# Kernel optimization log

Measured on AMD Instinct MI355X. Metric: run time of the kernel, lower is better.

The kernel has to match this reference:

```python
import jax, jax.numpy as jnp
import numpy as np

B, T, E, H = 1, 2048, 2048, 32
D = E // H  # head_dim = 64


def alibi_bias(n_heads, t_q, t_k, dtype):
    # slopes: 2^(-8*(h+1)/n_heads) for power-of-two head counts
    slopes = jnp.power(2.0, -8.0 * jnp.arange(1, n_heads + 1, dtype=jnp.float32) / n_heads)
    i = jnp.arange(t_q)[:, None] + (t_k - t_q)  # absolute query positions
    j = jnp.arange(t_k)[None, :]
    rel = (j - i).astype(dtype)                 # [t_q, t_k], <=0 on/below diagonal
    return (slopes[:, None, None] * rel).astype(dtype)  # [H, t_q, t_k]


def setup_inputs() -> dict:
    key = jax.random.key(0)
    kx, kq, kk, kv, ko = jax.random.split(key, 5)
    s = E ** -0.5
    x = jax.random.normal(kx, (B, T, E), dtype=jnp.float32)
    Wq = jax.random.normal(kq, (E, E), dtype=jnp.float32) * s
    Wk = jax.random.normal(kk, (D, E), dtype=jnp.float32) * s
    Wv = jax.random.normal(kv, (D, E), dtype=jnp.float32) * s
    Wo = jax.random.normal(ko, (E, E), dtype=jnp.float32) * s
    # causal mask: True where attention is disallowed (j > i)
    attention_mask = jnp.triu(jnp.ones((T, T), dtype=bool), k=1)[None, None]  # [1,1,T,T]
    return {"x": x, "Wq": Wq, "Wk": Wk, "Wv": Wv, "Wo": Wo, "attention_mask": attention_mask}


def reference(x, Wq, Wk, Wv, Wo, attention_mask):
    b, t, _ = x.shape
    scale = D ** -0.5
    q = (x @ Wq.T).reshape(b, t, H, D).transpose(0, 2, 1, 3)  # [b,H,t,D]
    k = x @ Wk.T                                              # [b,t,D] (single KV head)
    v = x @ Wv.T                                              # [b,t,D]
    attn = jnp.einsum('bhtd,bsd->bhts', q * scale, k)         # [b,H,t,t]
    attn = attn + alibi_bias(H, t, t, attn.dtype)[None]
    attn = jnp.where(attention_mask, jnp.asarray(-10000.0, attn.dtype), attn)
    w = jax.nn.softmax(attn, axis=-1)
    out = jnp.einsum('bhts,bsd->bhtd', w, v)                  # [b,H,t,D]
    out = out.transpose(0, 2, 1, 3).reshape(b, t, E)
    return out @ Wo.T
```

## Files before the change

kernel.cpp:

```cpp
#include <hip/hip_runtime.h>
#include <stdint.h>

typedef __bf16 bf16;
typedef __bf16 bf16x4 __attribute__((ext_vector_type(4)));
typedef __bf16 bf16x8 __attribute__((ext_vector_type(8)));
typedef short short4v __attribute__((ext_vector_type(4)));
typedef float floatx4 __attribute__((ext_vector_type(4)));

#define MFMA32(a, b, c) __builtin_amdgcn_mfma_f32_16x16x32_bf16((a), (b), (c), 0, 0, 0)

__device__ __forceinline__ floatx4 mfma16(bf16x4 a, bf16x4 b, floatx4 c) {
  return __builtin_amdgcn_mfma_f32_16x16x16bf16_1k(
      __builtin_bit_cast(short4v, a), __builtin_bit_cast(short4v, b), c, 0, 0, 0);
}

__device__ __forceinline__ void gload16(const void* g, void* l) {
  __builtin_amdgcn_global_load_lds(
      (const __attribute__((address_space(1))) void*)g,
      (__attribute__((address_space(3))) void*)l, 16, 0, 0);
}

__device__ __forceinline__ bf16x8 load8(const float* p) {
  float4 lo = *(const float4*)p;
  float4 hi = *(const float4*)(p + 4);
  bf16x8 r;
  r[0] = (bf16)lo.x; r[1] = (bf16)lo.y; r[2] = (bf16)lo.z; r[3] = (bf16)lo.w;
  r[4] = (bf16)hi.x; r[5] = (bf16)hi.y; r[6] = (bf16)hi.z; r[7] = (bf16)hi.w;
  return r;
}

__global__ __launch_bounds__(256) void conv3(const float* __restrict__ a, bf16* __restrict__ ab,
                                             const float* __restrict__ b, bf16* __restrict__ bb,
                                             const float* __restrict__ c, bf16* __restrict__ cb) {
  const int i = blockIdx.x * 256 + threadIdx.x;
  const float* src = blockIdx.y == 0 ? a : (blockIdx.y == 1 ? b : c);
  bf16* dst = blockIdx.y == 0 ? ab : (blockIdx.y == 1 ? bb : cb);
  ((bf16x8*)dst)[i] = load8(src + (size_t)i * 8);
}

__global__ __launch_bounds__(256) void pack_kv(const float* __restrict__ Kf,
                                               const float* __restrict__ Vf,
                                               bf16* __restrict__ Kb,
                                               bf16* __restrict__ Vtb) {
  int i = blockIdx.x * 256 + threadIdx.x;
  if (i < 2048 * 64) {
    Kb[i] = (bf16)Kf[i];
    const int t = i >> 6, d = i & 63;
    Vtb[(size_t)d * 2048 + t] = (bf16)Vf[i];
  }
}

template <typename TC>
__global__ __launch_bounds__(256) void gemm_bt_a(const bf16* __restrict__ A,
                                                 const bf16* __restrict__ B,
                                                 TC* __restrict__ C,
                                                 int M, int N, int K) {
  __shared__ __align__(16) bf16 As[2][64 * 32];
  __shared__ __align__(16) bf16 Bs[2][128 * 32];
  const int tid = threadIdx.x;
  const int wave = tid >> 6, lane = tid & 63;
  const int quad = lane >> 4, l16 = lane & 15;
  const int m0 = blockIdx.y * 64, n0 = blockIdx.x * 128;
  const int wm = (wave >> 1) * 32, wn = (wave & 1) * 64;

  floatx4 acc[2][4];
#pragma unroll
  for (int i = 0; i < 2; i++)
#pragma unroll
    for (int j = 0; j < 4; j++) acc[i][j] = (floatx4)0.f;

  const int srow = tid >> 2, scol = (tid & 3) * 8;
  const bf16* Ap = A + (size_t)(m0 + srow) * K + scol;
  const bf16* Bp = B + (size_t)(n0 + srow) * K + scol;

  auto stage = [&](int k0, int buf) {
    gload16(Ap + k0, (char*)As[buf] + tid * 16);
    gload16(Bp + k0, (char*)Bs[buf] + tid * 16);
    gload16(Bp + (size_t)64 * K + k0, (char*)Bs[buf] + 4096 + tid * 16);
  };
  auto compute = [&](int buf) {
    bf16x8 af[2], bfr[4];
#pragma unroll
    for (int mt = 0; mt < 2; mt++)
      af[mt] = *(const bf16x8*)(&As[buf][(wm + mt * 16 + l16) * 32 + quad * 8]);
#pragma unroll
    for (int nt = 0; nt < 4; nt++)
      bfr[nt] = *(const bf16x8*)(&Bs[buf][(wn + nt * 16 + l16) * 32 + quad * 8]);
#pragma unroll
    for (int mt = 0; mt < 2; mt++)
#pragma unroll
      for (int nt = 0; nt < 4; nt++)
        acc[mt][nt] = MFMA32(af[mt], bfr[nt], acc[mt][nt]);
  };

  stage(0, 0);
  for (int k0 = 0; k0 < K; k0 += 64) {
    __syncthreads();
    if (k0 + 32 < K) stage(k0 + 32, 1);
    compute(0);
    __syncthreads();
    if (k0 + 64 < K) stage(k0 + 64, 0);
    compute(1);
  }

#pragma unroll
  for (int mt = 0; mt < 2; mt++) {
#pragma unroll
    for (int nt = 0; nt < 4; nt++) {
      const int col = n0 + wn + nt * 16 + l16;
      const int row = m0 + wm + mt * 16 + quad * 4;
#pragma unroll
      for (int r = 0; r < 4; r++)
        C[(size_t)(row + r) * N + col] = (TC)acc[mt][nt][r];
    }
  }
}

__global__ __launch_bounds__(256) void kv_gemm(const bf16* __restrict__ xb,
                                               const float* __restrict__ Wk,
                                               const float* __restrict__ Wv,
                                               float* __restrict__ Kf,
                                               float* __restrict__ Vf) {
  __shared__ __align__(16) bf16 As[128 * 40];
  __shared__ __align__(16) bf16 Bs[128 * 40];
  const int tid = threadIdx.x;
  const int wave = tid >> 6, lane = tid & 63;
  const int quad = lane >> 4, l16 = lane & 15;
  const int m0 = blockIdx.y * 128;
  const int kbeg = blockIdx.x * 256, kend = kbeg + 256;
  const int wm = (wave >> 1) * 64, wn = (wave & 1) * 64;

  floatx4 acc[4][4];
#pragma unroll
  for (int i = 0; i < 4; i++)
#pragma unroll
    for (int j = 0; j < 4; j++) acc[i][j] = (floatx4)0.f;

  const int sr = tid >> 2, sc = (tid & 3) * 8;

  for (int k0 = kbeg; k0 < kend; k0 += 32) {
    __syncthreads();
#pragma unroll
    for (int rr = 0; rr < 2; rr++) {
      const int row = sr + rr * 64;
      *(bf16x8*)(&As[row * 40 + sc]) =
          *(const bf16x8*)(&xb[(size_t)(m0 + row) * 2048 + k0 + sc]);
      const float* bsrc = (row < 64) ? &Wk[(size_t)row * 2048 + k0 + sc]
                                     : &Wv[(size_t)(row - 64) * 2048 + k0 + sc];
      *(bf16x8*)(&Bs[row * 40 + sc]) = load8(bsrc);
    }
    __syncthreads();

    bf16x8 af[4], bfr[4];
#pragma unroll
    for (int mt = 0; mt < 4; mt++)
      af[mt] = *(const bf16x8*)(&As[(wm + mt * 16 + l16) * 40 + quad * 8]);
#pragma unroll
    for (int nt = 0; nt < 4; nt++)
      bfr[nt] = *(const bf16x8*)(&Bs[(wn + nt * 16 + l16) * 40 + quad * 8]);
#pragma unroll
    for (int mt = 0; mt < 4; mt++)
#pragma unroll
      for (int nt = 0; nt < 4; nt++)
        acc[mt][nt] = MFMA32(af[mt], bfr[nt], acc[mt][nt]);
  }

#pragma unroll
  for (int mt = 0; mt < 4; mt++) {
#pragma unroll
    for (int nt = 0; nt < 4; nt++) {
      const int col = wn + nt * 16 + l16;
      const int row = m0 + wm + mt * 16 + quad * 4;
      float* dst = (col < 64) ? &Kf[(size_t)row * 64 + col]
                              : &Vf[(size_t)row * 64 + (col - 64)];
#pragma unroll
      for (int r = 0; r < 4; r++) atomicAdd(dst + (size_t)r * 64, acc[mt][nt][r]);
    }
  }
}

__global__ __launch_bounds__(1024) void attn_kernel(const bf16* __restrict__ Q,
                                                    const bf16* __restrict__ Kb,
                                                    const bf16* __restrict__ Vtb,
                                                    bf16* __restrict__ O) {
  __shared__ __align__(16) char smem[65536];
  bf16* const Ksm = (bf16*)smem;
  bf16* const Vsm = (bf16*)(smem + 32768);
  float* const comb = (float*)smem;

  const int tid = threadIdx.x;
  const int wq = tid >> 6;
  const int grp = wq >> 3;
  const int wrow = wq & 7;
  const int lane = tid & 63;
  const int quad = lane >> 4, l16 = lane & 15;
  const int h = blockIdx.y;
  const int t = (blockIdx.y < 16) ? (15 - blockIdx.x) : blockIdx.x;
  const float scale2 = 0.125f * 1.44269504f;
  const float slope2 = exp2f(-0.25f * (float)(h + 1)) * 1.44269504f;

  float cq[4];
#pragma unroll
  for (int r = 0; r < 4; r++) cq[r] = slope2 * (float)(quad * 4 + r);
  const float s16 = slope2 * 16.f;
  const bf16x4 ones = {(bf16)1.f, (bf16)1.f, (bf16)1.f, (bf16)1.f};

  const int qi = t * 128 + wrow * 16 + l16;
  bf16x8 qf[2];
#pragma unroll
  for (int kk = 0; kk < 2; kk++)
    qf[kk] = *(const bf16x8*)(&Q[(size_t)qi * 2048 + h * 64 + kk * 32 + quad * 8]);

  floatx4 oacc[4];
#pragma unroll
  for (int dt = 0; dt < 4; dt++) oacc[dt] = (floatx4)0.f;
  floatx4 lacc = (floatx4)0.f;

  const int end = 2 * t + 2;
  const int lo_key = t * 128 - (int)(44.f / slope2);
  const int lo_t = (lo_key <= 0) ? 0 : (lo_key >> 6);
  const int n = (end - lo_t + 1) >> 1;
  const int base = lo_t + grp * n;
  const int kt_last = end - 1;
  const int qw0 = t * 128 + wrow * 16;

  const int tg = tid & 511;
  const int r0 = tg >> 3, sl = tg & 7;
  const int wsw = ((sl ^ (r0 & 7)) << 3);
  const int sx = l16 & 7;

  int kn = min(base, kt_last) * 64;
  bf16x8 kreg = *(const bf16x8*)(&Kb[(size_t)(kn + r0) * 64 + sl * 8]);
  bf16x8 vreg = *(const bf16x8*)(&Vtb[(size_t)r0 * 2048 + kn + sl * 8]);

  for (int i = 0; i < n; i++) {
    const int kt = base + i;
    const int bofs = (grp * 2 + (i & 1)) * 4096;
    *(bf16x8*)(&Ksm[bofs + r0 * 64 + wsw]) = kreg;
    *(bf16x8*)(&Vsm[bofs + r0 * 64 + wsw]) = vreg;
    __syncthreads();
    if (i + 1 < n) {
      const int kn2 = min(kt + 1, kt_last) * 64;
      kreg = *(const bf16x8*)(&Kb[(size_t)(kn2 + r0) * 64 + sl * 8]);
      vreg = *(const bf16x8*)(&Vtb[(size_t)r0 * 2048 + kn2 + sl * 8]);
    }
    const int k0 = kt * 64;
    if (kt >= end) continue;
    if (k0 > qw0 + 15) continue;
    if ((float)(qw0 - k0 - 63) * slope2 > 44.f) continue;

    const bf16* ks = Ksm + bofs;
    const bf16* vs = Vsm + bofs;

    floatx4 s[4];
#pragma unroll
    for (int mt = 0; mt < 4; mt++) s[mt] = (floatx4)0.f;
#pragma unroll
    for (int kk = 0; kk < 2; kk++) {
#pragma unroll
      for (int mt = 0; mt < 4; mt++) {
        bf16x8 kf = *(const bf16x8*)(
            &ks[(mt * 16 + l16) * 64 + (((kk * 4 + quad) ^ sx) << 3)]);
        s[mt] = MFMA32(kf, qf[kk], s[mt]);
      }
    }

    const float base0 = slope2 * (float)(k0 - qi);
    bf16x4 pb[4];
    if (k0 + 63 <= qw0) {
      float b = base0;
#pragma unroll
      for (int mt = 0; mt < 4; mt++) {
        bf16x4 tb;
#pragma unroll
        for (int r = 0; r < 4; r++)
          tb[r] = (bf16)exp2f(__builtin_fmaf(s[mt][r], scale2, b + cq[r]));
        pb[mt] = tb;
        b += s16;
      }
    } else {
      const int qloc = qi - k0;
      float b = base0;
#pragma unroll
      for (int mt = 0; mt < 4; mt++) {
        bf16x4 tb;
#pragma unroll
        for (int r = 0; r < 4; r++) {
          const int moff = mt * 16 + quad * 4 + r;
          const float p = exp2f(__builtin_fmaf(s[mt][r], scale2, b + cq[r]));
          tb[r] = (moff <= qloc) ? (bf16)p : (bf16)0.f;
        }
        pb[mt] = tb;
        b += s16;
      }
    }

#pragma unroll
    for (int mt = 0; mt < 4; mt++) {
      lacc = mfma16(ones, pb[mt], lacc);
#pragma unroll
      for (int dt = 0; dt < 4; dt++) {
        const int slot = 2 * mt + (quad >> 1);
        const bf16x4 va = *(const bf16x4*)(
            &vs[(dt * 16 + l16) * 64 + ((slot ^ sx) << 3) + (quad & 1) * 4]);
        oacc[dt] = mfma16(va, pb[mt], oacc[dt]);
      }
    }
  }

  __syncthreads();
  if (grp == 1) {
    float* c = comb + (size_t)(wrow * 64 + lane) * 17;
#pragma unroll
    for (int dt = 0; dt < 4; dt++)
#pragma unroll
      for (int r = 0; r < 4; r++) c[dt * 4 + r] = oacc[dt][r];
    c[16] = lacc[0];
  }
  __syncthreads();
  if (grp == 0) {
    const float* c = comb + (size_t)(wrow * 64 + lane) * 17;
    const float linv = 1.0f / (lacc[0] + c[16]);
#pragma unroll
    for (int dt = 0; dt < 4; dt++) {
      bf16x4 ob;
#pragma unroll
      for (int r = 0; r < 4; r++)
        ob[r] = (bf16)((oacc[dt][r] + c[dt * 4 + r]) * linv);
      *(bf16x4*)(&O[(size_t)qi * 2048 + h * 64 + dt * 16 + quad * 4]) = ob;
    }
  }
}

extern "C" void kernel_launch(void* const* d_in, const int* in_sizes, int n_in,
                              void* d_out, int out_size, void* d_ws,
                              size_t ws_size, hipStream_t stream) {
  (void)in_sizes; (void)n_in; (void)out_size; (void)ws_size;
  const float* x = (const float*)d_in[0];
  const float* Wq = (const float*)d_in[1];
  const float* Wk = (const float*)d_in[2];
  const float* Wv = (const float*)d_in[3];
  const float* Wo = (const float*)d_in[4];
  float* out = (float*)d_out;

  const size_t NE = (size_t)2048 * 2048;
  bf16* xb = (bf16*)d_ws;
  bf16* Wqb = xb + NE;
  bf16* Wob = Wqb + NE;
  bf16* Qb = Wob + NE;
  float* Kf = (float*)(Qb + NE);
  float* Vf = Kf + 2048 * 64;
  bf16* Kb = (bf16*)(Vf + 2048 * 64);
  bf16* Vtb = Kb + 2048 * 64;
  bf16* AO = xb;

  hipMemsetAsync(Kf, 0, 2 * 2048 * 64 * sizeof(float), stream);
  conv3<<<dim3(2048, 3), 256, 0, stream>>>(x, xb, Wq, Wqb, Wo, Wob);
  gemm_bt_a<bf16><<<dim3(16, 32), 256, 0, stream>>>(xb, Wqb, Qb, 2048, 2048, 2048);
  kv_gemm<<<dim3(8, 16), 256, 0, stream>>>(xb, Wk, Wv, Kf, Vf);
  pack_kv<<<512, 256, 0, stream>>>(Kf, Vf, Kb, Vtb);
  attn_kernel<<<dim3(16, 32), 1024, 0, stream>>>(Qb, Kb, Vtb, AO);
  gemm_bt_a<float><<<dim3(16, 32), 256, 0, stream>>>(AO, Wob, out, 2048, 2048, 2048);
}
```

Baseline: 246.1 us.

## Split attention across key chunks with atomic partial sums and separate normalize kernel

Replaces the 512-block, 1024-thread attention kernel (two wave groups splitting the key range and combining through shared memory) with a split-K style grid of up to 4096 blocks of 512 threads. Each block handles up to four 64-key tiles and atomically adds unnormalized output and row sums into fp32 workspace buffers. A new norm_o kernel then divides and converts to bf16. The aim is better load balance and occupancy across CUs, at the cost of two extra memsets, many float atomics, and an extra pass over a 16 MB fp32 buffer.

New measurement: 399.8 us. 1.62x slower.

```diff
diff --git a/kernel.cpp b/kernel.cpp
--- a/kernel.cpp
+++ b/kernel.cpp
@@ -1,5 +1,6 @@
 #include <hip/hip_runtime.h>
 #include <stdint.h>
+#include <math.h>
 
 typedef __bf16 bf16;
 typedef __bf16 bf16x4 __attribute__((ext_vector_type(4)));
@@ -179,33 +180,41 @@
   }
 }
 
-__global__ __launch_bounds__(1024) void attn_kernel(const bf16* __restrict__ Q,
-                                                    const bf16* __restrict__ Kb,
-                                                    const bf16* __restrict__ Vtb,
-                                                    bf16* __restrict__ O) {
-  __shared__ __align__(16) char smem[65536];
-  bf16* const Ksm = (bf16*)smem;
-  bf16* const Vsm = (bf16*)(smem + 32768);
-  float* const comb = (float*)smem;
+__global__ __launch_bounds__(512) void attn_kernel(const bf16* __restrict__ Q,
+                                                   const bf16* __restrict__ Kb,
+                                                   const bf16* __restrict__ Vtb,
+                                                   float* __restrict__ Opart,
+                                                   float* __restrict__ lpart) {
+  __shared__ __align__(16) bf16 Ks[2][64 * 64];
+  __shared__ __align__(16) bf16 Vt[2][64 * 64];
+
+  const int byr = 511 - (int)blockIdx.y;
+  const int h = byr >> 4;
+  const int t = byr & 15;
+  const float slope2 = exp2f(-0.25f * (float)(h + 1)) * 1.44269504f;
+  const int lo_key = t * 128 - (int)(44.f / slope2);
+  const int lo_t = (lo_key <= 0) ? 0 : (lo_key >> 6);
+  const int end = 2 * t + 2;
+  const int m = end - lo_t;
+  const int kbeg = lo_t + (int)blockIdx.x * 4;
+  int cnt = m - (int)blockIdx.x * 4;
+  if (cnt <= 0) return;
+  if (cnt > 4) cnt = 4;
 
   const int tid = threadIdx.x;
-  const int wq = tid >> 6;
-  const int grp = wq >> 3;
-  const int wrow = wq & 7;
+  const int wave = tid >> 6;
   const int lane = tid & 63;
   const int quad = lane >> 4, l16 = lane & 15;
-  const int h = blockIdx.y;
-  const int t = (blockIdx.y < 16) ? (15 - blockIdx.x) : blockIdx.x;
   const float scale2 = 0.125f * 1.44269504f;
-  const float slope2 = exp2f(-0.25f * (float)(h + 1)) * 1.44269504f;
+  const bf16x4 ones = {(bf16)1.f, (bf16)1.f, (bf16)1.f, (bf16)1.f};
 
   float cq[4];
 #pragma unroll
   for (int r = 0; r < 4; r++) cq[r] = slope2 * (float)(quad * 4 + r);
   const float s16 = slope2 * 16.f;
-  const bf16x4 ones = {(bf16)1.f, (bf16)1.f, (bf16)1.f, (bf16)1.f};
-
-  const int qi = t * 128 + wrow * 16 + l16;
+
+  const int qi = t * 128 + wave * 16 + l16;
+  const int qw0 = t * 128 + wave * 16;
   bf16x8 qf[2];
 #pragma unroll
   for (int kk = 0; kk < 2; kk++)
@@ -216,41 +225,31 @@
   for (int dt = 0; dt < 4; dt++) oacc[dt] = (floatx4)0.f;
   floatx4 lacc = (floatx4)0.f;
 
-  const int end = 2 * t + 2;
-  const int lo_key = t * 128 - (int)(44.f / slope2);
-  const int lo_t = (lo_key <= 0) ? 0 : (lo_key >> 6);
-  const int n = (end - lo_t + 1) >> 1;
-  const int base = lo_t + grp * n;
-  const int kt_last = end - 1;
-  const int qw0 = t * 128 + wrow * 16;
-
-  const int tg = tid & 511;
-  const int r0 = tg >> 3, sl = tg & 7;
+  const int r0 = tid >> 3, sl = tid & 7;
   const int wsw = ((sl ^ (r0 & 7)) << 3);
   const int sx = l16 & 7;
 
-  int kn = min(base, kt_last) * 64;
+  int kn = kbeg * 64;
   bf16x8 kreg = *(const bf16x8*)(&Kb[(size_t)(kn + r0) * 64 + sl * 8]);
   bf16x8 vreg = *(const bf16x8*)(&Vtb[(size_t)r0 * 2048 + kn + sl * 8]);
 
-  for (int i = 0; i < n; i++) {
-    const int kt = base + i;
-    const int bofs = (grp * 2 + (i & 1)) * 4096;
-    *(bf16x8*)(&Ksm[bofs + r0 * 64 + wsw]) = kreg;
-    *(bf16x8*)(&Vsm[bofs + r0 * 64 + wsw]) = vreg;
-    __syncthreads();
-    if (i + 1 < n) {
-      const int kn2 = min(kt + 1, kt_last) * 64;
+  for (int i = 0; i < cnt; i++) {
+    const int kt = kbeg + i;
+    const int buf = i & 1;
+    *(bf16x8*)(&Ks[buf][r0 * 64 + wsw]) = kreg;
+    *(bf16x8*)(&Vt[buf][r0 * 64 + wsw]) = vreg;
+    __syncthreads();
+    if (i + 1 < cnt) {
+      const int kn2 = (kt + 1) * 64;
       kreg = *(const bf16x8*)(&Kb[(size_t)(kn2 + r0) * 64 + sl * 8]);
       vreg = *(const bf16x8*)(&Vtb[(size_t)r0 * 2048 + kn2 + sl * 8]);
     }
     const int k0 = kt * 64;
-    if (kt >= end) continue;
     if (k0 > qw0 + 15) continue;
     if ((float)(qw0 - k0 - 63) * slope2 > 44.f) continue;
 
-    const bf16* ks = Ksm + bofs;
-    const bf16* vs = Vsm + bofs;
+    const bf16* ks = Ks[buf];
+    const bf16* vs = Vt[buf];
 
     floatx4 s[4];
 #pragma unroll
@@ -308,28 +307,30 @@
     }
   }
 
-  __syncthreads();
-  if (grp == 1) {
-    float* c = comb + (size_t)(wrow * 64 + lane) * 17;
-#pragma unroll
-    for (int dt = 0; dt < 4; dt++)
-#pragma unroll
-      for (int r = 0; r < 4; r++) c[dt * 4 + r] = oacc[dt][r];
-    c[16] = lacc[0];
-  }
-  __syncthreads();
-  if (grp == 0) {
-    const float* c = comb + (size_t)(wrow * 64 + lane) * 17;
-    const float linv = 1.0f / (lacc[0] + c[16]);
-#pragma unroll
-    for (int dt = 0; dt < 4; dt++) {
-      bf16x4 ob;
-#pragma unroll
-      for (int r = 0; r < 4; r++)
-        ob[r] = (bf16)((oacc[dt][r] + c[dt * 4 + r]) * linv);
-      *(bf16x4*)(&O[(size_t)qi * 2048 + h * 64 + dt * 16 + quad * 4]) = ob;
-    }
-  }
+  float* op = Opart + (size_t)qi * 2048 + h * 64;
+#pragma unroll
+  for (int dt = 0; dt < 4; dt++)
+#pragma unroll
+    for (int r = 0; r < 4; r++)
+      atomicAdd(op + dt * 16 + quad * 4 + r, oacc[dt][r]);
+  if (quad == 0) atomicAdd(&lpart[(size_t)qi * 32 + h], lacc[0]);
+}
+
+__global__ __launch_bounds__(256) void norm_o(const float* __restrict__ P,
+                                              const float* __restrict__ L,
+                                              bf16* __restrict__ AO) {
+  const int idx = blockIdx.x * 256 + threadIdx.x;
+  const int qi = idx >> 8;
+  const int cs = (idx & 255) << 3;
+  const float linv = 1.f / L[(size_t)qi * 32 + (cs >> 6)];
+  const float4 lo = *(const float4*)(P + (size_t)qi * 2048 + cs);
+  const float4 hi = *(const float4*)(P + (size_t)qi * 2048 + cs + 4);
+  bf16x8 o;
+  o[0] = (bf16)(lo.x * linv); o[1] = (bf16)(lo.y * linv);
+  o[2] = (bf16)(lo.z * linv); o[3] = (bf16)(lo.w * linv);
+  o[4] = (bf16)(hi.x * linv); o[5] = (bf16)(hi.y * linv);
+  o[6] = (bf16)(hi.z * linv); o[7] = (bf16)(hi.w * linv);
+  *(bf16x8*)(AO + (size_t)qi * 2048 + cs) = o;
 }
 
 extern "C" void kernel_launch(void* const* d_in, const int* in_sizes, int n_in,
@@ -352,13 +353,18 @@
   float* Vf = Kf + 2048 * 64;
   bf16* Kb = (bf16*)(Vf + 2048 * 64);
   bf16* Vtb = Kb + 2048 * 64;
-  bf16* AO = xb;
+  float* Opart = (float*)d_ws;
+  float* lpart = Kf;
+  bf16* AO = Qb;
 
   hipMemsetAsync(Kf, 0, 2 * 2048 * 64 * sizeof(float), stream);
   conv3<<<dim3(2048, 3), 256, 0, stream>>>(x, xb, Wq, Wqb, Wo, Wob);
   gemm_bt_a<bf16><<<dim3(16, 32), 256, 0, stream>>>(xb, Wqb, Qb, 2048, 2048, 2048);
   kv_gemm<<<dim3(8, 16), 256, 0, stream>>>(xb, Wk, Wv, Kf, Vf);
   pack_kv<<<512, 256, 0, stream>>>(Kf, Vf, Kb, Vtb);
-  attn_kernel<<<dim3(16, 32), 1024, 0, stream>>>(Qb, Kb, Vtb, AO);
+  hipMemsetAsync(Opart, 0, NE * sizeof(float), stream);
+  hipMemsetAsync(lpart, 0, (size_t)2048 * 32 * sizeof(float), stream);
+  attn_kernel<<<dim3(8, 512), 512, 0, stream>>>(Qb, Kb, Vtb, Opart, lpart);
+  norm_o<<<2048, 256, 0, stream>>>(Opart, lpart, AO);
   gemm_bt_a<float><<<dim3(16, 32), 256, 0, stream>>>(AO, Wob, out, 2048, 2048, 2048);
 }
```
